# Optimization experiments

Measured on AMD Instinct MI355X. Metric: run time of the kernel, lower is better.

## Reference

```python
import jax, jax.numpy as jnp
import numpy as np

N_NODES = 100000
N_EDGES = 1000000
N_REL = 7
IN_CH, HID_CH, OUT_CH = 128, 64, 2
N_BASES = 4  # used as num_blocks in layer 1, num_bases in layer 2


def setup_inputs() -> dict:
    key = jax.random.key(0)
    ks = jax.random.split(key, 10)
    x = jax.random.normal(ks[0], (N_NODES, IN_CH), dtype=jnp.float32)
    edge_index = jax.random.randint(ks[1], (2, N_EDGES), 0, N_NODES)
    edge_type = jax.random.randint(ks[2], (N_EDGES,), 0, N_REL)
    s = 0.05
    # layer 1: block-diagonal decomposition W1[r] is block-diag with B blocks
    W1 = jax.random.normal(ks[3], (N_REL, N_BASES, IN_CH // N_BASES, HID_CH // N_BASES), dtype=jnp.float32) * s
    root1 = jax.random.normal(ks[4], (IN_CH, HID_CH), dtype=jnp.float32) * s
    bias1 = jax.random.normal(ks[5], (HID_CH,), dtype=jnp.float32) * s
    # layer 2: basis decomposition W2[r] = sum_b comp2[r,b] * basis2[b]
    comp2 = jax.random.normal(ks[6], (N_REL, N_BASES), dtype=jnp.float32) * s
    basis2 = jax.random.normal(ks[7], (N_BASES, HID_CH, OUT_CH), dtype=jnp.float32) * s
    root2 = jax.random.normal(ks[8], (HID_CH, OUT_CH), dtype=jnp.float32) * s
    bias2 = jax.random.normal(ks[9], (OUT_CH,), dtype=jnp.float32) * s
    return {"x": x, "edge_index": edge_index, "edge_type": edge_type,
            "W1": W1, "root1": root1, "bias1": bias1,
            "comp2": comp2, "basis2": basis2, "root2": root2, "bias2": bias2}


def _relation_max_agg(msg, dst, edge_type, r, n_nodes):
    # segment-max over edges of relation r; empty segments -> 0 (PyG scatter-max behavior)
    seg = jnp.where(edge_type == r, dst, n_nodes)  # dump other relations into slot N
    agg = jax.ops.segment_max(msg, seg, num_segments=n_nodes + 1)[:n_nodes]
    deg = jax.ops.segment_sum(jnp.ones_like(seg, dtype=jnp.int32), seg, num_segments=n_nodes + 1)[:n_nodes]
    return jnp.where(deg[:, None] > 0, agg, 0.0)


def rgcn_conv_blocks(x, src, dst, edge_type, W, root, bias, n_nodes):
    # W: [R, B, in/B, out/B]  (block-diagonal weights)
    R, B, di, do = W.shape
    xb = x[src].reshape(-1, B, di)  # [E, B, in/B]
    out = x @ root + bias
    for r in range(R):
        msg = jnp.einsum('ebi,bio->ebo', xb, W[r]).reshape(-1, B * do)  # [E, out]
        out = out + _relation_max_agg(msg, dst, edge_type, r, n_nodes)
    return out


def rgcn_conv_bases(x, src, dst, edge_type, comp, basis, root, bias, n_nodes):
    # W[r] = sum_b comp[r,b] * basis[b]; basis: [B, in, out]
    W = jnp.einsum('rb,bio->rio', comp, basis)  # [R, in, out]
    xs = x[src]  # [E, in]
    out = x @ root + bias
    for r in range(W.shape[0]):
        msg = xs @ W[r]  # [E, out]
        out = out + _relation_max_agg(msg, dst, edge_type, r, n_nodes)
    return out


def reference(x, edge_index, edge_type, W1, root1, bias1, comp2, basis2, root2, bias2):
    src, dst = edge_index[0], edge_index[1]
    n = x.shape[0]
    h = rgcn_conv_blocks(x, src, dst, edge_type, W1, root1, bias1, n)
    h = jax.nn.relu(h)
    # dropout p=0.4 is identity in eval mode
    out = rgcn_conv_bases(h, src, dst, edge_type, comp2, basis2, root2, bias2, n)
    return out
```

## Files before the change

### kernel.cpp

```cpp
#include <hip/hip_runtime.h>

#define N_NODES 100000
#define N_EDGESV 1000000
#define N_REL 7
#define IN_CH 128
#define HID_CH 64
#define NBINS 800000
#define OFFM 0x0FFFFFFFu
#define NTILES 6250
#define NSB 196
#define SBCAP 8192
#define NBLK_A1 512
#define CHUNK 1954
#define XH_BLOCKS 2048
#define WB_BLOCKS 64
#define XH_TOTAL (N_NODES * IN_CH / 4)

typedef _Float16 f16;
typedef __attribute__((ext_vector_type(8))) _Float16 f16x8;
typedef __attribute__((ext_vector_type(4))) _Float16 f16x4;
typedef __attribute__((ext_vector_type(4))) float f32x4;

__global__ __launch_bounds__(256)
void k1_fused_kernel(const int* __restrict__ ei, const int* __restrict__ et,
                     int* __restrict__ gcur, int2* __restrict__ btmp,
                     const float* __restrict__ x, f16* __restrict__ xh,
                     const float* __restrict__ root1, const float* __restrict__ W1,
                     const float* __restrict__ comp2, const float* __restrict__ basis2,
                     const float* __restrict__ root2, f16* __restrict__ wbt,
                     f16* __restrict__ w2t)
{
    __shared__ int2 ent[CHUNK];
    __shared__ int lhist[NSB], lcur[NSB], gposl[NSB];
    const int bid = blockIdx.x;

    if (bid < NBLK_A1) {
        const int cbase = bid * CHUNK;
        const int cnt = min(CHUNK, N_EDGESV - cbase);

        for (int i = threadIdx.x; i < NSB; i += 256) { lhist[i] = 0; lcur[i] = 0; }
        __syncthreads();

        for (int i = threadIdx.x; i < cnt; i += 256) {
            int e = cbase + i;
            int d = ei[N_EDGESV + e];
            int s = ei[e];
            int r = et[e];
            ent[i] = make_int2((d << 3) + r, (s * 1024 + 128 + r * 128) | (r << 28));
            atomicAdd(&lhist[d >> 9], 1);
        }
        __syncthreads();

        for (int b = threadIdx.x; b < NSB; b += 256)
            gposl[b] = atomicAdd(&gcur[b], lhist[b]);
        __syncthreads();

        for (int i = threadIdx.x; i < cnt; i += 256) {
            int2 en = ent[i];
            int b = en.x >> 12;
            int off = atomicAdd(&lcur[b], 1);
            int idx = gposl[b] + off;
            if (idx < SBCAP) btmp[(size_t)b * SBCAP + idx] = en;
        }
    } else if (bid < NBLK_A1 + XH_BLOCKS) {
        for (int i = (bid - NBLK_A1) * 256 + threadIdx.x; i < XH_TOTAL;
             i += XH_BLOCKS * 256) {
            float4 v = ((const float4*)x)[i];
            f16x4 o = {(f16)v.x, (f16)v.y, (f16)v.z, (f16)v.w};
            *(f16x4*)(xh + (size_t)i * 4) = o;
        }
    } else {
        const int t0 = (bid - NBLK_A1 - XH_BLOCKS) * 256 + threadIdx.x;
        for (int idx = t0; idx < 512 * 128; idx += WB_BLOCKS * 256) {
            int p = idx >> 7, k = idx & 127;
            int lp = p & 63;
            int lc = ((lp & 15) >> 2) * 16 + ((lp >> 4) << 2) + (lp & 3);
            int col = (p & ~63) | lc;
            float v;
            if (col < 64) {
                v = root1[k * HID_CH + col];
            } else {
                int cc = col - 64, r = cc >> 6, inner = cc & 63, b = inner >> 4, j = inner & 15;
                int kb = k - b * 32;
                v = (kb >= 0 && kb < 32) ? W1[(((r * 4 + b) * 32) + kb) * 16 + j] : 0.f;
            }
            wbt[idx] = (f16)v;
        }
        for (int idx = t0; idx < 16 * 64; idx += WB_BLOCKS * 256) {
            int col = idx >> 6, k = idx & 63;
            float v;
            if (col < 14) {
                int r = col >> 1, oc = col & 1;
                v = 0.f;
                for (int b = 0; b < 4; ++b) v += comp2[r * 4 + b] * basis2[(b * 64 + k) * 2 + oc];
            } else {
                v = root2[k * 2 + (col - 14)];
            }
            w2t[idx] = (f16)v;
        }
    }
}

__global__ __launch_bounds__(512, 4)
void gemm1_kernel(const f16* __restrict__ xh, const f16* __restrict__ wbt,
                  f16* __restrict__ dense1) {
    const int lane = threadIdx.x & 63;
    const int wv = threadIdx.x >> 6;
    const int m = lane & 15;
    const int quad = lane >> 4;

    f16x8 bf[4][4];
#pragma unroll
    for (int t = 0; t < 4; ++t) {
        const f16* wc = wbt + (size_t)(wv * 64 + t * 16 + m) * 128 + quad * 8;
#pragma unroll
        for (int kk = 0; kk < 4; ++kk)
            bf[t][kk] = *(const f16x8*)(wc + kk * 32);
    }

    int tile = blockIdx.x;
    f16x8 a[4];
    if (tile < NTILES) {
        const f16* xrow = xh + (size_t)(tile * 16 + m) * 128 + quad * 8;
#pragma unroll
        for (int kk = 0; kk < 4; ++kk) a[kk] = *(const f16x8*)(xrow + kk * 32);
    }

    while (tile < NTILES) {
        const int n0 = tile * 16;
        const int next = tile + gridDim.x;

        f16x8 hv[2];
#pragma unroll
        for (int t = 0; t < 4; ++t) {
            f32x4 acc = {0.f, 0.f, 0.f, 0.f};
#pragma unroll
            for (int kk = 0; kk < 4; ++kk)
                acc = __builtin_amdgcn_mfma_f32_16x16x32_f16(bf[t][kk], a[kk], acc, 0, 0, 0);
#pragma unroll
            for (int i = 0; i < 4; ++i)
                hv[t >> 1][(t & 1) * 4 + i] = (f16)acc[i];
        }

        if (next < NTILES) {
            const f16* xrow = xh + (size_t)(next * 16 + m) * 128 + quad * 8;
#pragma unroll
            for (int kk = 0; kk < 4; ++kk) a[kk] = *(const f16x8*)(xrow + kk * 32);
        }

        f16* dst = dense1 + (size_t)(n0 + m) * 512 + wv * 64 + quad * 16;
        *(f16x8*)dst       = hv[0];
        *(f16x8*)(dst + 8) = hv[1];
        tile = next;
    }
}

__global__ __launch_bounds__(256)
void passA2_kernel(const int* __restrict__ gcur, const int2* __restrict__ btmp,
                   int* __restrict__ off2, int* __restrict__ packed1) {
    __shared__ int hist[4096];
    __shared__ int aux[256];
    __shared__ int shv[1];
    const int b = blockIdx.x >> 2;
    const int q = blockIdx.x & 3;
    const int t = threadIdx.x;

    if (blockIdx.x == 0 && t == 0) off2[0] = 0;

    int v0 = (t < NSB) ? min(gcur[t], SBCAP) : 0;
    aux[t] = v0;
    __syncthreads();
    for (int d = 1; d < 256; d <<= 1) {
        int xv = (t >= d) ? aux[t - d] : 0;
        __syncthreads();
        if (t >= d) aux[t] += xv;
        __syncthreads();
    }
    if (t == 0) shv[0] = (b == 0) ? 0 : aux[b - 1];
    __syncthreads();
    const int gb = shv[0];
    const int cnt = min(gcur[b], SBCAP);
    const int2* base = btmp + (size_t)b * SBCAP;
    __syncthreads();

    for (int i = t; i < 4096; i += 256) hist[i] = 0;
    __syncthreads();
    for (int i = t; i < cnt; i += 256) atomicAdd(&hist[base[i].x & 4095], 1);
    __syncthreads();

    int loc[16];
    int run = 0;
#pragma unroll
    for (int j = 0; j < 16; ++j) { loc[j] = run; run += hist[t * 16 + j]; }
    aux[t] = run;
    __syncthreads();
    for (int d = 1; d < 256; d <<= 1) {
        int xv = (t >= d) ? aux[t - d] : 0;
        __syncthreads();
        if (t >= d) aux[t] += xv;
        __syncthreads();
    }
    const int tbase = aux[t] - run;
    __syncthreads();

#pragma unroll
    for (int j = 0; j < 16; ++j) {
        int bin = t * 16 + j;
        int excl = tbase + loc[j];
        int incl = excl + hist[bin];
        if ((t >> 6) == q) {
            int gkey = (b << 12) + bin;
            if (gkey < NBINS) off2[gkey + 1] = gb + incl;
        }
        hist[bin] = excl;
    }
    __syncthreads();

    for (int i = t; i < cnt; i += 256) {
        int2 e = base[i];
        int lb = e.x & 4095;
        if ((lb >> 10) == q) {
            int pos = gb + atomicAdd(&hist[lb], 1);
            packed1[pos] = e.y;
        }
    }
}

__global__ __launch_bounds__(256)
void agg1_kernel(const f16* __restrict__ dense1, const float* __restrict__ bias1,
                 const int* __restrict__ off2, const int* __restrict__ packed1,
                 f16* __restrict__ h16)
{
    const int lane = threadIdx.x & 63;
    const int lane2 = lane * 2;
    const char* m1 = (const char*)dense1;
    const int wid = blockIdx.x * 4 + (threadIdx.x >> 6);
    const int nw = gridDim.x * 4;
    const float bias = bias1[lane];

    for (int n = wid; n < N_NODES; n += nw) {
        const int st = off2[n << 3];
        const int en = off2[(n << 3) + 7];
        const float hroot = (float)dense1[(size_t)n * 512 + lane];
        float add = 0.f, cur = 0.f;
        int prev_r = -1;

#define MRG(kk, vv) { \
        int r_ = (int)((kk) >> 28); \
        bool same_ = (r_ == prev_r); \
        add += same_ ? 0.f : cur; \
        cur = same_ ? fmaxf(cur, (vv)) : (vv); \
        prev_r = r_; }

        int p = st;
        for (; p + 7 < en; p += 8) {
            unsigned k0 = (unsigned)packed1[p];
            unsigned k1 = (unsigned)packed1[p + 1];
            unsigned k2 = (unsigned)packed1[p + 2];
            unsigned k3 = (unsigned)packed1[p + 3];
            unsigned k4 = (unsigned)packed1[p + 4];
            unsigned k5 = (unsigned)packed1[p + 5];
            unsigned k6 = (unsigned)packed1[p + 6];
            unsigned k7 = (unsigned)packed1[p + 7];
            float v0 = (float)*(const f16*)(m1 + (k0 & OFFM) + lane2);
            float v1 = (float)*(const f16*)(m1 + (k1 & OFFM) + lane2);
            float v2 = (float)*(const f16*)(m1 + (k2 & OFFM) + lane2);
            float v3 = (float)*(const f16*)(m1 + (k3 & OFFM) + lane2);
            float v4 = (float)*(const f16*)(m1 + (k4 & OFFM) + lane2);
            float v5 = (float)*(const f16*)(m1 + (k5 & OFFM) + lane2);
            float v6 = (float)*(const f16*)(m1 + (k6 & OFFM) + lane2);
            float v7 = (float)*(const f16*)(m1 + (k7 & OFFM) + lane2);
            MRG(k0, v0) MRG(k1, v1) MRG(k2, v2) MRG(k3, v3)
            MRG(k4, v4) MRG(k5, v5) MRG(k6, v6) MRG(k7, v7)
        }
        for (; p + 3 < en; p += 4) {
            unsigned k0 = (unsigned)packed1[p];
            unsigned k1 = (unsigned)packed1[p + 1];
            unsigned k2 = (unsigned)packed1[p + 2];
            unsigned k3 = (unsigned)packed1[p + 3];
            float v0 = (float)*(const f16*)(m1 + (k0 & OFFM) + lane2);
            float v1 = (float)*(const f16*)(m1 + (k1 & OFFM) + lane2);
            float v2 = (float)*(const f16*)(m1 + (k2 & OFFM) + lane2);
            float v3 = (float)*(const f16*)(m1 + (k3 & OFFM) + lane2);
            MRG(k0, v0) MRG(k1, v1) MRG(k2, v2) MRG(k3, v3)
        }
        for (; p < en; ++p) {
            unsigned k0 = (unsigned)packed1[p];
            float v0 = (float)*(const f16*)(m1 + (k0 & OFFM) + lane2);
            MRG(k0, v0)
        }
#undef MRG
        add += cur;

        h16[((size_t)n << 6) + lane] = (f16)fmaxf(hroot + bias + add, 0.f);
    }
}

__global__ __launch_bounds__(256)
void pre2_kernel(const f16* __restrict__ h16, const f16* __restrict__ w2t,
                 const float* __restrict__ bias2, float* __restrict__ msg2) {
    const int lane = threadIdx.x & 63;
    const int wv = threadIdx.x >> 6;
    const int nt = blockIdx.x * 4 + wv;
    if (nt >= NTILES) return;
    const int n0 = nt * 16;
    const int m = lane & 15;
    const int quad = lane >> 4;

    const f16* hrow = h16 + (size_t)(n0 + m) * 64 + quad * 8;
    const f16* wcol = w2t + (size_t)m * 64 + quad * 8;
    f32x4 acc = {0.f, 0.f, 0.f, 0.f};
    f16x8 a0 = *(const f16x8*)(hrow);
    f16x8 b0 = *(const f16x8*)(wcol);
    acc = __builtin_amdgcn_mfma_f32_16x16x32_f16(a0, b0, acc, 0, 0, 0);
    f16x8 a1 = *(const f16x8*)(hrow + 32);
    f16x8 b1 = *(const f16x8*)(wcol + 32);
    acc = __builtin_amdgcn_mfma_f32_16x16x32_f16(a1, b1, acc, 0, 0, 0);

    const float badd = (m == 14) ? bias2[0] : ((m == 15) ? bias2[1] : 0.f);
#pragma unroll
    for (int i = 0; i < 4; ++i)
        msg2[(size_t)(n0 + quad * 4 + i) * 16 + m] = acc[i] + badd;
}

__global__ __launch_bounds__(256)
void agg2_kernel(const float* __restrict__ msg2, const int* __restrict__ off2,
                 const int* __restrict__ packed1, float* __restrict__ out)
{
    const int n = blockIdx.x * blockDim.x + threadIdx.x;
    if (n >= N_NODES) return;
    const char* m2 = (const char*)msg2;
    const int st = off2[n << 3];
    const int en = off2[(n << 3) + 7];
    float addx = 0.f, addy = 0.f, curx = 0.f, cury = 0.f;
    int prev_r = -1;

#define MRG2(kk, ff) { \
    int r_ = (int)((kk) >> 28); \
    bool same_ = (r_ == prev_r); \
    addx += same_ ? 0.f : curx; \
    addy += same_ ? 0.f : cury; \
    curx = same_ ? fmaxf(curx, (ff).x) : (ff).x; \
    cury = same_ ? fmaxf(cury, (ff).y) : (ff).y; \
    prev_r = r_; }

    int p = st;
    for (; p + 7 < en; p += 8) {
        unsigned k0 = (unsigned)packed1[p],     k1 = (unsigned)packed1[p + 1];
        unsigned k2 = (unsigned)packed1[p + 2], k3 = (unsigned)packed1[p + 3];
        unsigned k4 = (unsigned)packed1[p + 4], k5 = (unsigned)packed1[p + 5];
        unsigned k6 = (unsigned)packed1[p + 6], k7 = (unsigned)packed1[p + 7];
        float2 f0 = *(const float2*)(m2 + (((k0 & OFFM) >> 4) - 8));
        float2 f1 = *(const float2*)(m2 + (((k1 & OFFM) >> 4) - 8));
        float2 f2 = *(const float2*)(m2 + (((k2 & OFFM) >> 4) - 8));
        float2 f3 = *(const float2*)(m2 + (((k3 & OFFM) >> 4) - 8));
        float2 f4 = *(const float2*)(m2 + (((k4 & OFFM) >> 4) - 8));
        float2 f5 = *(const float2*)(m2 + (((k5 & OFFM) >> 4) - 8));
        float2 f6 = *(const float2*)(m2 + (((k6 & OFFM) >> 4) - 8));
        float2 f7 = *(const float2*)(m2 + (((k7 & OFFM) >> 4) - 8));
        MRG2(k0, f0) MRG2(k1, f1) MRG2(k2, f2) MRG2(k3, f3)
        MRG2(k4, f4) MRG2(k5, f5) MRG2(k6, f6) MRG2(k7, f7)
    }
    for (; p < en; ++p) {
        unsigned k0 = (unsigned)packed1[p];
        float2 f0 = *(const float2*)(m2 + (((k0 & OFFM) >> 4) - 8));
        MRG2(k0, f0)
    }
#undef MRG2

    out[(size_t)n * 2 + 0] = msg2[(size_t)n * 16 + 14] + addx + curx;
    out[(size_t)n * 2 + 1] = msg2[(size_t)n * 16 + 15] + addy + cury;
}

extern "C" void kernel_launch(void* const* d_in, const int* in_sizes, int n_in,
                              void* d_out, int out_size, void* d_ws, size_t ws_size,
                              hipStream_t stream)
{
    const float* x      = (const float*)d_in[0];
    const int*   ei     = (const int*)d_in[1];
    const int*   et     = (const int*)d_in[2];
    const float* W1     = (const float*)d_in[3];
    const float* root1  = (const float*)d_in[4];
    const float* bias1  = (const float*)d_in[5];
    const float* comp2  = (const float*)d_in[6];
    const float* basis2 = (const float*)d_in[7];
    const float* root2  = (const float*)d_in[8];
    const float* bias2  = (const float*)d_in[9];
    float* out = (float*)d_out;

    char* ws = (char*)d_ws;
    size_t o = 0;
    auto carve = [&](size_t bytes) { char* p = ws + o; o += (bytes + 255) & ~(size_t)255; return p; };
    int*   off2    = (int*)carve(sizeof(int) * (NBINS + 1));
    int*   gcur    = (int*)carve(sizeof(int) * NSB);
    int2*  btmp    = (int2*)carve(sizeof(int2) * (size_t)NSB * SBCAP);
    int*   packed1 = (int*)carve(sizeof(int) * N_EDGESV);
    f16*   xh      = (f16*)carve(sizeof(f16) * (size_t)N_NODES * IN_CH);
    f16*   wbt     = (f16*)carve(sizeof(f16) * 512 * 128);
    f16*   w2t     = (f16*)carve(sizeof(f16) * 16 * 64);
    f16*   dense1  = (f16*)carve(sizeof(f16) * (size_t)N_NODES * 512);
    f16*   h16     = (f16*)carve(sizeof(f16) * (size_t)N_NODES * HID_CH);
    float* msg2    = (float*)carve(sizeof(float) * (size_t)N_NODES * 16);

    hipMemsetAsync(gcur, 0, sizeof(int) * NSB, stream);

    k1_fused_kernel<<<NBLK_A1 + XH_BLOCKS + WB_BLOCKS, 256, 0, stream>>>(
        ei, et, gcur, btmp, x, xh, root1, W1, comp2, basis2, root2, wbt, w2t);

    gemm1_kernel<<<1024, 512, 0, stream>>>(xh, wbt, dense1);

    passA2_kernel<<<NSB * 4, 256, 0, stream>>>(gcur, btmp, off2, packed1);

    agg1_kernel<<<2048, 256, 0, stream>>>(dense1, bias1, off2, packed1, h16);

    pre2_kernel<<<(NTILES + 3) / 4, 256, 0, stream>>>(h16, w2t, bias2, msg2);
    agg2_kernel<<<(N_NODES + 255) / 256, 256, 0, stream>>>(msg2, off2, packed1, out);
}
```

Before: 262.4 us.

## Fuse all six stages into one cooperative persistent kernel with grid syncs

Replaces the memset and six separate kernel launches with a single cooperative kernel of 512 blocks × 512 threads, separating the stages with grid.sync(). The intent is to remove per-launch overhead and inter-kernel gaps. The cost is that each phase is confined to a fixed persistent grid, so per-phase occupancy and parallelism can drop. The cooperative launch may also fail if 512 blocks cannot be co-resident, in which case the old multi-kernel path runs as a fallback.

```diff
diff --git a/kernel.cpp b/kernel.cpp
--- a/kernel.cpp
+++ b/kernel.cpp
@@ -1,4 +1,5 @@
 #include <hip/hip_runtime.h>
+#include <hip/hip_cooperative_groups.h>
 
 #define N_NODES 100000
 #define N_EDGESV 1000000
@@ -15,11 +16,365 @@
 #define XH_BLOCKS 2048
 #define WB_BLOCKS 64
 #define XH_TOTAL (N_NODES * IN_CH / 4)
+#define MB 512
+#define MT 512
 
 typedef _Float16 f16;
 typedef __attribute__((ext_vector_type(8))) _Float16 f16x8;
 typedef __attribute__((ext_vector_type(4))) _Float16 f16x4;
 typedef __attribute__((ext_vector_type(4))) float f32x4;
+
+__global__ __launch_bounds__(MT, 4)
+void mega_kernel(const int* __restrict__ ei, const int* __restrict__ et,
+                 const float* __restrict__ x, const float* __restrict__ W1,
+                 const float* __restrict__ root1, const float* __restrict__ bias1,
+                 const float* __restrict__ comp2, const float* __restrict__ basis2,
+                 const float* __restrict__ root2, const float* __restrict__ bias2,
+                 int* __restrict__ gcur, int2* __restrict__ btmp,
+                 int* __restrict__ off2, int* __restrict__ packed1,
+                 f16* __restrict__ xh, f16* __restrict__ wbt, f16* __restrict__ w2t,
+                 f16* __restrict__ dense1, f16* __restrict__ h16,
+                 float* __restrict__ msg2, float* __restrict__ out)
+{
+    cooperative_groups::grid_group grid = cooperative_groups::this_grid();
+    __shared__ __align__(16) char smem[18944];
+    const int tid = threadIdx.x;
+    const int bid = blockIdx.x;
+    const int gtid = bid * MT + tid;
+
+    if (gtid < NSB) gcur[gtid] = 0;
+    if (gtid == NSB) off2[0] = 0;
+    for (int i = gtid; i < XH_TOTAL; i += MB * MT) {
+        float4 v = ((const float4*)x)[i];
+        f16x4 o = {(f16)v.x, (f16)v.y, (f16)v.z, (f16)v.w};
+        *(f16x4*)(xh + (size_t)i * 4) = o;
+    }
+    for (int idx = gtid; idx < 512 * 128; idx += MB * MT) {
+        int p = idx >> 7, k = idx & 127;
+        int lp = p & 63;
+        int lc = ((lp & 15) >> 2) * 16 + ((lp >> 4) << 2) + (lp & 3);
+        int col = (p & ~63) | lc;
+        float v;
+        if (col < 64) {
+            v = root1[k * HID_CH + col];
+        } else {
+            int cc = col - 64, r = cc >> 6, inner = cc & 63, b = inner >> 4, j = inner & 15;
+            int kb = k - b * 32;
+            v = (kb >= 0 && kb < 32) ? W1[(((r * 4 + b) * 32) + kb) * 16 + j] : 0.f;
+        }
+        wbt[idx] = (f16)v;
+    }
+    for (int idx = gtid; idx < 16 * 64; idx += MB * MT) {
+        int col = idx >> 6, k = idx & 63;
+        float v;
+        if (col < 14) {
+            int r = col >> 1, oc = col & 1;
+            v = 0.f;
+            for (int b = 0; b < 4; ++b) v += comp2[r * 4 + b] * basis2[(b * 64 + k) * 2 + oc];
+        } else {
+            v = root2[k * 2 + (col - 14)];
+        }
+        w2t[idx] = (f16)v;
+    }
+    grid.sync();
+
+    {
+        int2* ent  = (int2*)smem;
+        int* lhist = (int*)(smem + 15632);
+        int* lcur  = (int*)(smem + 16416);
+        int* gposl = (int*)(smem + 17200);
+        const int cbase = bid * CHUNK;
+        const int cnt = min(CHUNK, N_EDGESV - cbase);
+
+        for (int i = tid; i < NSB; i += MT) { lhist[i] = 0; lcur[i] = 0; }
+        __syncthreads();
+
+        for (int i = tid; i < cnt; i += MT) {
+            int e = cbase + i;
+            int d = ei[N_EDGESV + e];
+            int s = ei[e];
+            int r = et[e];
+            ent[i] = make_int2((d << 3) + r, (s * 1024 + 128 + r * 128) | (r << 28));
+            atomicAdd(&lhist[d >> 9], 1);
+        }
+        __syncthreads();
+
+        for (int b = tid; b < NSB; b += MT)
+            gposl[b] = atomicAdd(&gcur[b], lhist[b]);
+        __syncthreads();
+
+        for (int i = tid; i < cnt; i += MT) {
+            int2 en = ent[i];
+            int b = en.x >> 12;
+            int off = atomicAdd(&lcur[b], 1);
+            int idx = gposl[b] + off;
+            if (idx < SBCAP) btmp[(size_t)b * SBCAP + idx] = en;
+        }
+    }
+    grid.sync();
+
+    {
+        int* hist = (int*)smem;
+        int* aux  = (int*)(smem + 16384);
+        int* shv  = (int*)(smem + 18432);
+        for (int rid = bid; rid < NSB * 4; rid += MB) {
+            __syncthreads();
+            const int b = rid >> 2;
+            const int q = rid & 3;
+            const int t = tid;
+
+            int v = (t < NSB) ? min(gcur[t], SBCAP) : 0;
+            aux[t] = v;
+            __syncthreads();
+            for (int d = 1; d < 256; d <<= 1) {
+                int xv = (t >= d) ? aux[t - d] : 0;
+                __syncthreads();
+                if (t >= d) aux[t] += xv;
+                __syncthreads();
+            }
+            if (t == 0) shv[0] = (b == 0) ? 0 : aux[b - 1];
+            __syncthreads();
+            const int gb = shv[0];
+            const int cnt = min(gcur[b], SBCAP);
+            const int2* base = btmp + (size_t)b * SBCAP;
+            __syncthreads();
+
+            for (int i = t; i < 4096; i += MT) hist[i] = 0;
+            __syncthreads();
+            for (int i = t; i < cnt; i += MT) atomicAdd(&hist[base[i].x & 4095], 1);
+            __syncthreads();
+
+            int loc[8];
+            int run = 0;
+#pragma unroll
+            for (int j = 0; j < 8; ++j) { loc[j] = run; run += hist[t * 8 + j]; }
+            aux[t] = run;
+            __syncthreads();
+            for (int d = 1; d < 512; d <<= 1) {
+                int xv = (t >= d) ? aux[t - d] : 0;
+                __syncthreads();
+                if (t >= d) aux[t] += xv;
+                __syncthreads();
+            }
+            const int tbase = aux[t] - run;
+            __syncthreads();
+
+#pragma unroll
+            for (int j = 0; j < 8; ++j) {
+                int bin = t * 8 + j;
+                int excl = tbase + loc[j];
+                int incl = excl + hist[bin];
+                if ((t >> 7) == q) {
+                    int gkey = (b << 12) + bin;
+                    if (gkey < NBINS) off2[gkey + 1] = gb + incl;
+                }
+                hist[bin] = excl;
+            }
+            __syncthreads();
+
+            for (int i = t; i < cnt; i += MT) {
+                int2 e = base[i];
+                int lb = e.x & 4095;
+                if ((lb >> 10) == q) {
+                    int pos = gb + atomicAdd(&hist[lb], 1);
+                    packed1[pos] = e.y;
+                }
+            }
+        }
+    }
+    grid.sync();
+
+    {
+        const int lane = tid & 63;
+        const int wv = tid >> 6;
+        const int m = lane & 15;
+        const int quad = lane >> 4;
+
+        f16x8 bf[4][4];
+#pragma unroll
+        for (int t = 0; t < 4; ++t) {
+            const f16* wc = wbt + (size_t)(wv * 64 + t * 16 + m) * 128 + quad * 8;
+#pragma unroll
+            for (int kk = 0; kk < 4; ++kk)
+                bf[t][kk] = *(const f16x8*)(wc + kk * 32);
+        }
+
+        int tile = bid;
+        f16x8 a[4];
+        if (tile < NTILES) {
+            const f16* xrow = xh + (size_t)(tile * 16 + m) * 128 + quad * 8;
+#pragma unroll
+            for (int kk = 0; kk < 4; ++kk) a[kk] = *(const f16x8*)(xrow + kk * 32);
+        }
+
+        while (tile < NTILES) {
+            const int n0 = tile * 16;
+            const int next = tile + MB;
+
+            f16x8 hv[2];
+#pragma unroll
+            for (int t = 0; t < 4; ++t) {
+                f32x4 acc = {0.f, 0.f, 0.f, 0.f};
+#pragma unroll
+                for (int kk = 0; kk < 4; ++kk)
+                    acc = __builtin_amdgcn_mfma_f32_16x16x32_f16(bf[t][kk], a[kk], acc, 0, 0, 0);
+#pragma unroll
+                for (int i = 0; i < 4; ++i)
+                    hv[t >> 1][(t & 1) * 4 + i] = (f16)acc[i];
+            }
+
+            if (next < NTILES) {
+                const f16* xrow = xh + (size_t)(next * 16 + m) * 128 + quad * 8;
+#pragma unroll
+                for (int kk = 0; kk < 4; ++kk) a[kk] = *(const f16x8*)(xrow + kk * 32);
+            }
+
+            f16* dst = dense1 + (size_t)(n0 + m) * 512 + wv * 64 + quad * 16;
+            *(f16x8*)dst       = hv[0];
+            *(f16x8*)(dst + 8) = hv[1];
+            tile = next;
+        }
+    }
+    grid.sync();
+
+    {
+        const int lane = tid & 63;
+        const int lane2 = lane * 2;
+        const char* m1 = (const char*)dense1;
+        const int wid = bid * 8 + (tid >> 6);
+        const int nw = MB * 8;
+        const float bias = bias1[lane];
+
+        for (int n = wid; n < N_NODES; n += nw) {
+            const int st = off2[n << 3];
+            const int en = off2[(n << 3) + 7];
+            const float hroot = (float)dense1[(size_t)n * 512 + lane];
+            float add = 0.f, cur = 0.f;
+            int prev_r = -1;
+
+#define MRG(kk, vv) { \
+            int r_ = (int)((kk) >> 28); \
+            bool same_ = (r_ == prev_r); \
+            add += same_ ? 0.f : cur; \
+            cur = same_ ? fmaxf(cur, (vv)) : (vv); \
+            prev_r = r_; }
+
+            int p = st;
+            for (; p + 7 < en; p += 8) {
+                unsigned k0 = (unsigned)packed1[p];
+                unsigned k1 = (unsigned)packed1[p + 1];
+                unsigned k2 = (unsigned)packed1[p + 2];
+                unsigned k3 = (unsigned)packed1[p + 3];
+                unsigned k4 = (unsigned)packed1[p + 4];
+                unsigned k5 = (unsigned)packed1[p + 5];
+                unsigned k6 = (unsigned)packed1[p + 6];
+                unsigned k7 = (unsigned)packed1[p + 7];
+                float v0 = (float)*(const f16*)(m1 + (k0 & OFFM) + lane2);
+                float v1 = (float)*(const f16*)(m1 + (k1 & OFFM) + lane2);
+                float v2 = (float)*(const f16*)(m1 + (k2 & OFFM) + lane2);
+                float v3 = (float)*(const f16*)(m1 + (k3 & OFFM) + lane2);
+                float v4 = (float)*(const f16*)(m1 + (k4 & OFFM) + lane2);
+                float v5 = (float)*(const f16*)(m1 + (k5 & OFFM) + lane2);
+                float v6 = (float)*(const f16*)(m1 + (k6 & OFFM) + lane2);
+                float v7 = (float)*(const f16*)(m1 + (k7 & OFFM) + lane2);
+                MRG(k0, v0) MRG(k1, v1) MRG(k2, v2) MRG(k3, v3)
+                MRG(k4, v4) MRG(k5, v5) MRG(k6, v6) MRG(k7, v7)
+            }
+            for (; p + 3 < en; p += 4) {
+                unsigned k0 = (unsigned)packed1[p];
+                unsigned k1 = (unsigned)packed1[p + 1];
+                unsigned k2 = (unsigned)packed1[p + 2];
+                unsigned k3 = (unsigned)packed1[p + 3];
+                float v0 = (float)*(const f16*)(m1 + (k0 & OFFM) + lane2);
+                float v1 = (float)*(const f16*)(m1 + (k1 & OFFM) + lane2);
+                float v2 = (float)*(const f16*)(m1 + (k2 & OFFM) + lane2);
+                float v3 = (float)*(const f16*)(m1 + (k3 & OFFM) + lane2);
+                MRG(k0, v0) MRG(k1, v1) MRG(k2, v2) MRG(k3, v3)
+            }
+            for (; p < en; ++p) {
+                unsigned k0 = (unsigned)packed1[p];
+                float v0 = (float)*(const f16*)(m1 + (k0 & OFFM) + lane2);
+                MRG(k0, v0)
+            }
+#undef MRG
+            add += cur;
+
+            h16[((size_t)n << 6) + lane] = (f16)fmaxf(hroot + bias + add, 0.f);
+        }
+    }
+    grid.sync();
+
+    {
+        const int lane = tid & 63;
+        const int wv = tid >> 6;
+        const int m = lane & 15;
+        const int quad = lane >> 4;
+        for (int nt = bid * 8 + wv; nt < NTILES; nt += MB * 8) {
+            const int n0 = nt * 16;
+            const f16* hrow = h16 + (size_t)(n0 + m) * 64 + quad * 8;
+            const f16* wcol = w2t + (size_t)m * 64 + quad * 8;
+            f32x4 acc = {0.f, 0.f, 0.f, 0.f};
+            f16x8 a0 = *(const f16x8*)(hrow);
+            f16x8 b0 = *(const f16x8*)(wcol);
+            acc = __builtin_amdgcn_mfma_f32_16x16x32_f16(a0, b0, acc, 0, 0, 0);
+            f16x8 a1 = *(const f16x8*)(hrow + 32);
+            f16x8 b1 = *(const f16x8*)(wcol + 32);
+            acc = __builtin_amdgcn_mfma_f32_16x16x32_f16(a1, b1, acc, 0, 0, 0);
+
+            const float badd = (m == 14) ? bias2[0] : ((m == 15) ? bias2[1] : 0.f);
+#pragma unroll
+            for (int i = 0; i < 4; ++i)
+                msg2[(size_t)(n0 + quad * 4 + i) * 16 + m] = acc[i] + badd;
+        }
+    }
+    grid.sync();
+
+    {
+        const char* m2 = (const char*)msg2;
+        for (int n = gtid; n < N_NODES; n += MB * MT) {
+            const int st = off2[n << 3];
+            const int en = off2[(n << 3) + 7];
+            float addx = 0.f, addy = 0.f, curx = 0.f, cury = 0.f;
+            int prev_r = -1;
+
+#define MRG2(kk, ff) { \
+            int r_ = (int)((kk) >> 28); \
+            bool same_ = (r_ == prev_r); \
+            addx += same_ ? 0.f : curx; \
+            addy += same_ ? 0.f : cury; \
+            curx = same_ ? fmaxf(curx, (ff).x) : (ff).x; \
+            cury = same_ ? fmaxf(cury, (ff).y) : (ff).y; \
+            prev_r = r_; }
+
+            int p = st;
+            for (; p + 7 < en; p += 8) {
+                unsigned k0 = (unsigned)packed1[p],     k1 = (unsigned)packed1[p + 1];
+                unsigned k2 = (unsigned)packed1[p + 2], k3 = (unsigned)packed1[p + 3];
+                unsigned k4 = (unsigned)packed1[p + 4], k5 = (unsigned)packed1[p + 5];
+                unsigned k6 = (unsigned)packed1[p + 6], k7 = (unsigned)packed1[p + 7];
+                float2 f0 = *(const float2*)(m2 + (((k0 & OFFM) >> 4) - 8));
+                float2 f1 = *(const float2*)(m2 + (((k1 & OFFM) >> 4) - 8));
+                float2 f2 = *(const float2*)(m2 + (((k2 & OFFM) >> 4) - 8));
+                float2 f3 = *(const float2*)(m2 + (((k3 & OFFM) >> 4) - 8));
+                float2 f4 = *(const float2*)(m2 + (((k4 & OFFM) >> 4) - 8));
+                float2 f5 = *(const float2*)(m2 + (((k5 & OFFM) >> 4) - 8));
+                float2 f6 = *(const float2*)(m2 + (((k6 & OFFM) >> 4) - 8));
+                float2 f7 = *(const float2*)(m2 + (((k7 & OFFM) >> 4) - 8));
+                MRG2(k0, f0) MRG2(k1, f1) MRG2(k2, f2) MRG2(k3, f3)
+                MRG2(k4, f4) MRG2(k5, f5) MRG2(k6, f6) MRG2(k7, f7)
+            }
+            for (; p < en; ++p) {
+                unsigned k0 = (unsigned)packed1[p];
+                float2 f0 = *(const float2*)(m2 + (((k0 & OFFM) >> 4) - 8));
+                MRG2(k0, f0)
+            }
+#undef MRG2
+
+            out[(size_t)n * 2 + 0] = msg2[(size_t)n * 16 + 14] + addx + curx;
+            out[(size_t)n * 2 + 1] = msg2[(size_t)n * 16 + 15] + addy + cury;
+        }
+    }
+}
 
 __global__ __launch_bounds__(256)
 void k1_fused_kernel(const int* __restrict__ ei, const int* __restrict__ et,
@@ -376,9 +731,9 @@
                               void* d_out, int out_size, void* d_ws, size_t ws_size,
                               hipStream_t stream)
 {
-    const float* x      = (const float*)d_in[0];
     const int*   ei     = (const int*)d_in[1];
     const int*   et     = (const int*)d_in[2];
+    const float* x      = (const float*)d_in[0];
     const float* W1     = (const float*)d_in[3];
     const float* root1  = (const float*)d_in[4];
     const float* bias1  = (const float*)d_in[5];
@@ -402,17 +757,23 @@
     f16*   h16     = (f16*)carve(sizeof(f16) * (size_t)N_NODES * HID_CH);
     float* msg2    = (float*)carve(sizeof(float) * (size_t)N_NODES * 16);
 
+    void* args[] = {
+        (void*)&ei, (void*)&et, (void*)&x, (void*)&W1, (void*)&root1, (void*)&bias1,
+        (void*)&comp2, (void*)&basis2, (void*)&root2, (void*)&bias2,
+        (void*)&gcur, (void*)&btmp, (void*)&off2, (void*)&packed1,
+        (void*)&xh, (void*)&wbt, (void*)&w2t, (void*)&dense1, (void*)&h16,
+        (void*)&msg2, (void*)&out
+    };
+    hipError_t err = hipLaunchCooperativeKernel(mega_kernel, dim3(MB), dim3(MT),
+                                                args, 0, stream);
+    if (err == hipSuccess) return;
+
     hipMemsetAsync(gcur, 0, sizeof(int) * NSB, stream);
-
     k1_fused_kernel<<<NBLK_A1 + XH_BLOCKS + WB_BLOCKS, 256, 0, stream>>>(
         ei, et, gcur, btmp, x, xh, root1, W1, comp2, basis2, root2, wbt, w2t);
-
     gemm1_kernel<<<1024, 512, 0, stream>>>(xh, wbt, dense1);
-
     passA2_kernel<<<NSB * 4, 256, 0, stream>>>(gcur, btmp, off2, packed1);
-
     agg1_kernel<<<2048, 256, 0, stream>>>(dense1, bias1, off2, packed1, h16);
-
     pre2_kernel<<<(NTILES + 3) / 4, 256, 0, stream>>>(h16, w2t, bias2, msg2);
     agg2_kernel<<<(N_NODES + 255) / 256, 256, 0, stream>>>(msg2, off2, packed1, out);
 }
```

Result: slower. 664.5 us (+153.3%).
